# Kernel optimization log

Hardware: AMD Instinct MI355X
Metric: run time of the kernel (lower is better)

Reference implementation:

```python
import jax, jax.numpy as jnp
import numpy as np

B, S, I, H, P = 4096, 1024, 6, 128, 50  # batch, seq_len, input_size, hidden_size, predict_size


def setup_inputs() -> dict:
    key = jax.random.key(0)
    ks = jax.random.split(key, 12)
    k = 1.0 / np.sqrt(H)  # torch LSTM default init: U(-1/sqrt(H), 1/sqrt(H))
    u = lambda kk, shape: jax.random.uniform(kk, shape, jnp.float32, -k, k)
    # xavier_uniform for fc: bound = sqrt(6/(fan_in+fan_out))
    xb = np.sqrt(6.0 / (H + I))
    return {
        "x": jax.random.normal(ks[0], (B, S, I), jnp.float32),
        "w_ih0": u(ks[1], (4 * H, I)),
        "w_hh0": u(ks[2], (4 * H, H)),
        "b_ih0": u(ks[3], (4 * H,)),
        "b_hh0": u(ks[4], (4 * H,)),
        "w_ih1": u(ks[5], (4 * H, H)),
        "w_hh1": u(ks[6], (4 * H, H)),
        "b_ih1": u(ks[7], (4 * H,)),
        "b_hh1": u(ks[8], (4 * H,)),
        "fc_w": jax.random.uniform(ks[9], (I, H), jnp.float32, -xb, xb),
        "fc_b": jnp.full((I,), 0.01, jnp.float32),
    }


def _cell(xt, h, c, w_ih, w_hh, b):
    # gates: [i, f, g, o] stacked along last dim (torch order)
    g = xt @ w_ih.T + h @ w_hh.T + b
    i, f, gg, o = jnp.split(g, 4, axis=-1)
    c = jax.nn.sigmoid(f) * c + jax.nn.sigmoid(i) * jnp.tanh(gg)
    h = jax.nn.sigmoid(o) * jnp.tanh(c)
    return h, c


def reference(x, w_ih0, w_hh0, b_ih0, b_hh0, w_ih1, w_hh1, b_ih1, b_hh1, fc_w, fc_b):
    b0 = b_ih0 + b_hh0
    b1 = b_ih1 + b_hh1
    z = jnp.zeros((x.shape[0], H), x.dtype)

    def two_layer_step(carry, xt):
        h0, c0, h1, c1 = carry
        h0, c0 = _cell(xt, h0, c0, w_ih0, w_hh0, b0)
        h1, c1 = _cell(h0, h1, c1, w_ih1, w_hh1, b1)
        return (h0, c0, h1, c1), None

    # encode the input sequence; last top-layer output == final h1
    (h0, c0, h1, c1), _ = jax.lax.scan(two_layer_step, (z, z, z, z),
                                       jnp.swapaxes(x, 0, 1))  # (S,B,I)
    cur = jnp.tanh(h1 @ fc_w.T + fc_b)  # (B, I)

    def ar_step(carry, _):
        h0, c0, h1, c1, cur = carry
        h0, c0 = _cell(cur, h0, c0, w_ih0, w_hh0, b0)
        h1, c1 = _cell(h0, h1, c1, w_ih1, w_hh1, b1)
        pred = jnp.tanh(h1 @ fc_w.T + fc_b)
        return (h0, c0, h1, c1, pred), pred

    _, preds = jax.lax.scan(ar_step, (h0, c0, h1, c1, cur), None, length=P)
    return jnp.swapaxes(preds, 0, 1)  # (B, P, I)
```

## Files before the change

kernel.cpp:

```cpp
#include <hip/hip_runtime.h>

#define SEQ 1024
#define ISZ 6
#define HSZ 128
#define PRED 50
#define MROW 16
#define HP   136
#define FP   132
#define XSLOT 180

using f32x4  = __attribute__((ext_vector_type(4))) float;
using bf16x8 = __attribute__((ext_vector_type(8))) short;

__device__ __forceinline__ short f2bf(float f){
  union { float f; unsigned u; } v; v.f = f;
  unsigned r = v.u + 0x7FFFu + ((v.u >> 16) & 1u);
  return (short)(r >> 16);
}
__device__ __forceinline__ float sigf(float x){
  float e = __builtin_amdgcn_exp2f(x * -1.4426950408889634f);
  return __builtin_amdgcn_rcpf(1.0f + e);
}
__device__ __forceinline__ float tanhf_(float x){
  float e = __builtin_amdgcn_exp2f(x * 2.8853900817779268f);
  return 1.0f - 2.0f * __builtin_amdgcn_rcpf(1.0f + e);
}

#define PIN(v) asm volatile("" : "+v"(v))

__global__
__attribute__((amdgpu_flat_work_group_size(512, 512)))
void lstm_ar(
    const float* __restrict__ x,
    const float* __restrict__ w_ih0, const float* __restrict__ w_hh0,
    const float* __restrict__ b_ih0, const float* __restrict__ b_hh0,
    const float* __restrict__ w_ih1, const float* __restrict__ w_hh1,
    const float* __restrict__ b_ih1, const float* __restrict__ b_hh1,
    const float* __restrict__ fc_w, const float* __restrict__ fc_b,
    float* __restrict__ out)
{
  __shared__ short s_h0[2][MROW*HP];
  __shared__ short s_h1[2][MROW*HP];
  __shared__ short s_x[XSLOT*MROW*8];
  __shared__ short s_wih0[512*8];
  __shared__ float s_h1f[MROW*FP];
  __shared__ float s_fcw[ISZ*HSZ];
  __shared__ float s_fcb[8];
  __shared__ short s_zpad[8];

  const int tid  = threadIdx.x;
  const int wv   = tid >> 6;
  const int lane = tid & 63;
  const int l15  = lane & 15;
  const int lq   = lane >> 4;
  const int U    = wv * 16;
  const int u    = U + l15;
  const int row0 = blockIdx.x * MROW;

  {
    short* p0 = &s_h0[0][0];
    short* p1 = &s_h1[0][0];
    for (int i = tid; i < 2*MROW*HP; i += 512){ p0[i] = 0; p1[i] = 0; }
    for (int i = tid; i < 65*MROW*8; i += 512) s_x[i] = 0;
    if (tid < 8){ s_zpad[tid] = 0; s_fcb[tid] = (tid < 6) ? fc_b[tid] : 0.f; }
    for (int i = tid; i < ISZ*HSZ; i += 512) s_fcw[i] = fc_w[i];
    {
      #pragma unroll
      for (int k = 0; k < 6; k++) s_wih0[tid*8 + k] = f2bf(w_ih0[tid*6 + k]);
      s_wih0[tid*8 + 6] = 0; s_wih0[tid*8 + 7] = 0;
    }
  }

  bf16x8 whh0f[4][4], wih1f[4][4], whh1f[4][4];
  float bias0[4], bias1[4];
  #pragma unroll
  for (int g = 0; g < 4; g++){
    const int c = g*128 + u;
    bias0[g] = b_ih0[c] + b_hh0[c];
    bias1[g] = b_ih1[c] + b_hh1[c];
    #pragma unroll
    for (int kt = 0; kt < 4; kt++){
      const int off = c*HSZ + kt*32 + lq*8;
      bf16x8 r0, r1, r2;
      #pragma unroll
      for (int i = 0; i < 8; i++){
        r0[i] = f2bf(w_hh0[off + i]);
        r1[i] = f2bf(w_ih1[off + i]);
        r2[i] = f2bf(w_hh1[off + i]);
      }
      whh0f[g][kt] = r0; wih1f[g][kt] = r1; whh1f[g][kt] = r2;
    }
  }

  float c0[4] = {0.f,0.f,0.f,0.f}, c1[4] = {0.f,0.f,0.f,0.f};
  __syncthreads();

  for (int t = 0; t < SEQ + PRED; ++t){
    #pragma unroll
    for (int g = 0; g < 4; g++){
      #pragma unroll
      for (int kt = 0; kt < 4; kt++){
        PIN(whh0f[g][kt]); PIN(wih1f[g][kt]); PIN(whh1f[g][kt]);
      }
    }

    if (t < SEQ && (t & 63) == 0){
      for (int i = tid; i < MROW*64*ISZ; i += 512){
        const int r   = i / (64*ISZ);
        const int rem = i % (64*ISZ);
        const int ts  = rem / ISZ;
        const int k   = rem % ISZ;
        const float v = x[(size_t)(row0 + r)*(SEQ*ISZ) + (size_t)(t + ts)*ISZ + k];
        s_x[(ts*MROW + r)*8 + k] = f2bf(v);
      }
      __syncthreads();
    }
    const int tt = (t < SEQ) ? (t & 63) : 64;
    const int pb = t & 1, qb = pb ^ 1;

    const short* pax = (lq == 0) ? (s_x + (tt*MROW + l15)*8) : s_zpad;
    const bf16x8 ax = *(const bf16x8*)pax;

    f32x4 acc[4];
    #pragma unroll
    for (int g = 0; g < 4; g++){
      const short* pw = (lq == 0) ? (s_wih0 + (g*128 + u)*8) : s_zpad;
      const bf16x8 bw = *(const bf16x8*)pw;
      f32x4 ci; ci[0] = bias0[g]; ci[1] = bias0[g]; ci[2] = bias0[g]; ci[3] = bias0[g];
      acc[g] = __builtin_amdgcn_mfma_f32_16x16x32_bf16(ax, bw, ci, 0, 0, 0);
    }
    #pragma unroll
    for (int kt = 0; kt < 4; kt++){
      const int s = kt*4 + lq;
      const short* pa = s_h0[qb] + l15*HP + s*8;
      const bf16x8 a = *(const bf16x8*)pa;
      #pragma unroll
      for (int g = 0; g < 4; g++)
        acc[g] = __builtin_amdgcn_mfma_f32_16x16x32_bf16(a, whh0f[g][kt], acc[g], 0, 0, 0);
    }
    #pragma unroll
    for (int j = 0; j < 4; j++){
      const float iv = sigf(acc[0][j]);
      const float fv = sigf(acc[1][j]);
      const float gv = tanhf_(acc[2][j]);
      const float ov = sigf(acc[3][j]);
      c0[j] = fv*c0[j] + iv*gv;
      const float h = ov * tanhf_(c0[j]);
      const int r = lq*4 + j;
      s_h0[pb][r*HP + u] = f2bf(h);
    }
    __syncthreads();

    #pragma unroll
    for (int g = 0; g < 4; g++){
      acc[g][0] = bias1[g]; acc[g][1] = bias1[g]; acc[g][2] = bias1[g]; acc[g][3] = bias1[g];
    }
    #pragma unroll
    for (int kt = 0; kt < 4; kt++){
      const int s = kt*4 + lq;
      const short* pa = s_h0[pb] + l15*HP + s*8;
      const bf16x8 a = *(const bf16x8*)pa;
      #pragma unroll
      for (int g = 0; g < 4; g++)
        acc[g] = __builtin_amdgcn_mfma_f32_16x16x32_bf16(a, wih1f[g][kt], acc[g], 0, 0, 0);
    }
    #pragma unroll
    for (int kt = 0; kt < 4; kt++){
      const int s = kt*4 + lq;
      const short* pa = s_h1[qb] + l15*HP + s*8;
      const bf16x8 a = *(const bf16x8*)pa;
      #pragma unroll
      for (int g = 0; g < 4; g++)
        acc[g] = __builtin_amdgcn_mfma_f32_16x16x32_bf16(a, whh1f[g][kt], acc[g], 0, 0, 0);
    }
    const bool dofc = (t >= SEQ - 1);
    #pragma unroll
    for (int j = 0; j < 4; j++){
      const float iv = sigf(acc[0][j]);
      const float fv = sigf(acc[1][j]);
      const float gv = tanhf_(acc[2][j]);
      const float ov = sigf(acc[3][j]);
      c1[j] = fv*c1[j] + iv*gv;
      const float h = ov * tanhf_(c1[j]);
      const int r = lq*4 + j;
      s_h1[pb][r*HP + u] = f2bf(h);
      if (dofc) s_h1f[r*FP + u] = h;
    }
    __syncthreads();

    if (dofc){
      if (tid < 96){
        const int r  = tid / 6;
        const int ii = tid % 6;
        const f32x4* hv = (const f32x4*)(s_h1f + r*FP);
        const f32x4* wf = (const f32x4*)(s_fcw + ii*128);
        float sacc = 0.f;
        #pragma unroll
        for (int kk = 0; kk < 32; kk++){
          const f32x4 a = hv[kk], b = wf[kk];
          sacc += a[0]*b[0] + a[1]*b[1] + a[2]*b[2] + a[3]*b[3];
        }
        const float pred = tanhf_(s_fcb[ii] + sacc);
        s_x[(64*MROW + r)*8 + ii] = f2bf(pred);
        if (t >= SEQ)
          out[(size_t)(row0 + r)*(PRED*ISZ) + (size_t)(t - SEQ)*ISZ + ii] = pred;
      }
      __syncthreads();
    }
  }
}

extern "C" void kernel_launch(void* const* d_in, const int* in_sizes, int n_in,
                              void* d_out, int out_size, void* d_ws, size_t ws_size,
                              hipStream_t stream) {
  const float* x     = (const float*)d_in[0];
  const float* w_ih0 = (const float*)d_in[1];
  const float* w_hh0 = (const float*)d_in[2];
  const float* b_ih0 = (const float*)d_in[3];
  const float* b_hh0 = (const float*)d_in[4];
  const float* w_ih1 = (const float*)d_in[5];
  const float* w_hh1 = (const float*)d_in[6];
  const float* b_ih1 = (const float*)d_in[7];
  const float* b_hh1 = (const float*)d_in[8];
  const float* fc_w  = (const float*)d_in[9];
  const float* fc_b  = (const float*)d_in[10];
  float* out = (float*)d_out;

  const int Btot = in_sizes[0] / (SEQ * ISZ);
  const int nblk = Btot / MROW;

  lstm_ar<<<dim3(nblk), dim3(512), 0, stream>>>(
      x, w_ih0, w_hh0, b_ih0, b_hh0, w_ih1, w_hh1, b_ih1, b_hh1, fc_w, fc_b, out);
}
```

Baseline: 3.675 ms.

## Move LSTM recurrent weights out of registers into LDS and workspace

Only w_ih1 stays register-resident. w_hh1 is converted to bf16 and stored in a 128 KB XOR-swizzled LDS array read on every step. w_hh0 is pre-converted to bf16 in a global workspace and re-streamed each step, with a fallback that reconverts from fp32 when no workspace is available. Biases move to LDS, the x staging chunk shrinks from 64 to 8 steps, and the FC reads bf16 h1 from LDS with fc_w from global. The aim is to cut register pressure, at the cost of extra LDS and global traffic on the serial critical path, a single-buffered h1 that needs an added barrier each step, and lower FC precision.

Result: faster. 3.207 ms (-12.7%).

```diff
diff --git a/kernel.cpp b/kernel.cpp
--- a/kernel.cpp
+++ b/kernel.cpp
@@ -6,8 +6,8 @@
 #define PRED 50
 #define MROW 16
 #define HP   136
-#define FP   132
-#define XSLOT 180
+#define XCH  8
+#define WSB  131072
 
 using f32x4  = __attribute__((ext_vector_type(4))) float;
 using bf16x8 = __attribute__((ext_vector_type(8))) short;
@@ -17,6 +17,9 @@
   unsigned r = v.u + 0x7FFFu + ((v.u >> 16) & 1u);
   return (short)(r >> 16);
 }
+__device__ __forceinline__ float bf2f(unsigned short us){
+  union { unsigned u; float f; } v; v.u = ((unsigned)us) << 16; return v.f;
+}
 __device__ __forceinline__ float sigf(float x){
   float e = __builtin_amdgcn_exp2f(x * -1.4426950408889634f);
   return __builtin_amdgcn_rcpf(1.0f + e);
@@ -28,6 +31,7 @@
 
 #define PIN(v) asm volatile("" : "+v"(v))
 
+template<int PRECVT>
 __global__
 __attribute__((amdgpu_flat_work_group_size(512, 512)))
 void lstm_ar(
@@ -37,14 +41,14 @@
     const float* __restrict__ w_ih1, const float* __restrict__ w_hh1,
     const float* __restrict__ b_ih1, const float* __restrict__ b_hh1,
     const float* __restrict__ fc_w, const float* __restrict__ fc_b,
-    float* __restrict__ out)
+    float* __restrict__ out, unsigned short* __restrict__ wsb)
 {
+  __shared__ short s_whh1[65536];
   __shared__ short s_h0[2][MROW*HP];
-  __shared__ short s_h1[2][MROW*HP];
-  __shared__ short s_x[XSLOT*MROW*8];
+  __shared__ short s_h1[MROW*HP];
+  __shared__ short s_x[(XCH+1)*MROW*8];
   __shared__ short s_wih0[512*8];
-  __shared__ float s_h1f[MROW*FP];
-  __shared__ float s_fcw[ISZ*HSZ];
+  __shared__ float s_bias[2*512];
   __shared__ float s_fcb[8];
   __shared__ short s_zpad[8];
 
@@ -53,90 +57,111 @@
   const int lane = tid & 63;
   const int l15  = lane & 15;
   const int lq   = lane >> 4;
-  const int U    = wv * 16;
-  const int u    = U + l15;
+  const int u    = wv*16 + l15;
   const int row0 = blockIdx.x * MROW;
-
+  char* const whh1b = (char*)s_whh1;
+
+  for (int i = tid; i < 2*MROW*HP; i += 512) (&s_h0[0][0])[i] = 0;
+  for (int i = tid; i < MROW*HP;   i += 512) s_h1[i] = 0;
+  for (int i = tid; i < (XCH+1)*MROW*8; i += 512) s_x[i] = 0;
+  if (tid < 8){ s_zpad[tid] = 0; s_fcb[tid] = (tid < 6) ? fc_b[tid] : 0.f; }
   {
-    short* p0 = &s_h0[0][0];
-    short* p1 = &s_h1[0][0];
-    for (int i = tid; i < 2*MROW*HP; i += 512){ p0[i] = 0; p1[i] = 0; }
-    for (int i = tid; i < 65*MROW*8; i += 512) s_x[i] = 0;
-    if (tid < 8){ s_zpad[tid] = 0; s_fcb[tid] = (tid < 6) ? fc_b[tid] : 0.f; }
-    for (int i = tid; i < ISZ*HSZ; i += 512) s_fcw[i] = fc_w[i];
-    {
-      #pragma unroll
-      for (int k = 0; k < 6; k++) s_wih0[tid*8 + k] = f2bf(w_ih0[tid*6 + k]);
-      s_wih0[tid*8 + 6] = 0; s_wih0[tid*8 + 7] = 0;
-    }
-  }
-
-  bf16x8 whh0f[4][4], wih1f[4][4], whh1f[4][4];
-  float bias0[4], bias1[4];
+    #pragma unroll
+    for (int k = 0; k < 6; k++) s_wih0[tid*8 + k] = f2bf(w_ih0[tid*6 + k]);
+    s_wih0[tid*8 + 6] = 0; s_wih0[tid*8 + 7] = 0;
+  }
+  for (int i = tid; i < 1024; i += 512)
+    s_bias[i] = (i < 512) ? (b_ih0[i] + b_hh0[i]) : (b_ih1[i-512] + b_hh1[i-512]);
+
+  for (int i = tid; i < 32768; i += 512){
+    const int c = i >> 6, kp = i & 63;
+    const unsigned lo = (unsigned short)f2bf(w_hh1[c*128 + 2*kp]);
+    const unsigned hi = (unsigned short)f2bf(w_hh1[c*128 + 2*kp + 1]);
+    *(unsigned*)(whh1b + ((i*4) ^ ((c & 7) << 4))) = lo | (hi << 16);
+  }
+
+  if (PRECVT){
+    #pragma unroll
+    for (int g = 0; g < 4; g++){
+      const int c = g*128 + u;
+      #pragma unroll
+      for (int kt = 0; kt < 4; kt++){
+        const float* wp = w_hh0 + c*HSZ + kt*32 + lq*8;
+        bf16x8 f;
+        #pragma unroll
+        for (int i = 0; i < 8; i++) f[i] = f2bf(wp[i]);
+        *(bf16x8*)(wsb + (((wv*4 + g)*4 + kt)*64 + lane)*8) = f;
+      }
+    }
+  }
+
+  bf16x8 wih1f[4][4];
   #pragma unroll
   for (int g = 0; g < 4; g++){
     const int c = g*128 + u;
-    bias0[g] = b_ih0[c] + b_hh0[c];
-    bias1[g] = b_ih1[c] + b_hh1[c];
-    #pragma unroll
-    for (int kt = 0; kt < 4; kt++){
-      const int off = c*HSZ + kt*32 + lq*8;
-      bf16x8 r0, r1, r2;
-      #pragma unroll
-      for (int i = 0; i < 8; i++){
-        r0[i] = f2bf(w_hh0[off + i]);
-        r1[i] = f2bf(w_ih1[off + i]);
-        r2[i] = f2bf(w_hh1[off + i]);
-      }
-      whh0f[g][kt] = r0; wih1f[g][kt] = r1; whh1f[g][kt] = r2;
+    #pragma unroll
+    for (int kt = 0; kt < 4; kt++){
+      const float* wp = w_ih1 + c*HSZ + kt*32 + lq*8;
+      bf16x8 f;
+      #pragma unroll
+      for (int i = 0; i < 8; i++) f[i] = f2bf(wp[i]);
+      wih1f[g][kt] = f;
     }
   }
 
   float c0[4] = {0.f,0.f,0.f,0.f}, c1[4] = {0.f,0.f,0.f,0.f};
+  volatile const float* vb = s_bias;
   __syncthreads();
 
   for (int t = 0; t < SEQ + PRED; ++t){
     #pragma unroll
     for (int g = 0; g < 4; g++){
       #pragma unroll
-      for (int kt = 0; kt < 4; kt++){
-        PIN(whh0f[g][kt]); PIN(wih1f[g][kt]); PIN(whh1f[g][kt]);
-      }
-    }
-
-    if (t < SEQ && (t & 63) == 0){
-      for (int i = tid; i < MROW*64*ISZ; i += 512){
-        const int r   = i / (64*ISZ);
-        const int rem = i % (64*ISZ);
-        const int ts  = rem / ISZ;
-        const int k   = rem % ISZ;
-        const float v = x[(size_t)(row0 + r)*(SEQ*ISZ) + (size_t)(t + ts)*ISZ + k];
-        s_x[(ts*MROW + r)*8 + k] = f2bf(v);
+      for (int kt = 0; kt < 4; kt++) PIN(wih1f[g][kt]);
+    }
+
+    if (t < SEQ && (t & (XCH-1)) == 0){
+      for (int i = tid; i < XCH*MROW*ISZ; i += 512){
+        const int r = i / (XCH*ISZ), rem = i % (XCH*ISZ);
+        const int ts = rem / ISZ, k = rem % ISZ;
+        s_x[(ts*MROW + r)*8 + k] =
+          f2bf(x[(size_t)(row0 + r)*(SEQ*ISZ) + (size_t)(t + ts)*ISZ + k]);
       }
       __syncthreads();
     }
-    const int tt = (t < SEQ) ? (t & 63) : 64;
+    const int tt = (t < SEQ) ? (t & (XCH-1)) : XCH;
     const int pb = t & 1, qb = pb ^ 1;
 
-    const short* pax = (lq == 0) ? (s_x + (tt*MROW + l15)*8) : s_zpad;
-    const bf16x8 ax = *(const bf16x8*)pax;
-
+    const bf16x8 ax = *(const bf16x8*)((lq == 0) ? (s_x + (tt*MROW + l15)*8) : s_zpad);
     f32x4 acc[4];
     #pragma unroll
     for (int g = 0; g < 4; g++){
-      const short* pw = (lq == 0) ? (s_wih0 + (g*128 + u)*8) : s_zpad;
-      const bf16x8 bw = *(const bf16x8*)pw;
-      f32x4 ci; ci[0] = bias0[g]; ci[1] = bias0[g]; ci[2] = bias0[g]; ci[3] = bias0[g];
+      const bf16x8 bw = *(const bf16x8*)((lq == 0) ? (s_wih0 + (g*128 + u)*8) : s_zpad);
+      const float bg = vb[g*128 + u];
+      f32x4 ci; ci[0] = bg; ci[1] = bg; ci[2] = bg; ci[3] = bg;
       acc[g] = __builtin_amdgcn_mfma_f32_16x16x32_bf16(ax, bw, ci, 0, 0, 0);
     }
     #pragma unroll
     for (int kt = 0; kt < 4; kt++){
-      const int s = kt*4 + lq;
-      const short* pa = s_h0[qb] + l15*HP + s*8;
-      const bf16x8 a = *(const bf16x8*)pa;
+      bf16x8 stg[4];
+      if (PRECVT){
+        #pragma unroll
+        for (int g = 0; g < 4; g++)
+          stg[g] = *(const bf16x8*)(wsb + (((wv*4 + g)*4 + kt)*64 + lane)*8);
+      } else {
+        #pragma unroll
+        for (int g = 0; g < 4; g++){
+          const float* wp = w_hh0 + (g*128 + u)*HSZ + kt*32 + lq*8;
+          bf16x8 f;
+          #pragma unroll
+          for (int i = 0; i < 8; i++) f[i] = f2bf(wp[i]);
+          stg[g] = f;
+        }
+      }
+      const bf16x8 a = *(const bf16x8*)(s_h0[qb] + l15*HP + (kt*4 + lq)*8);
       #pragma unroll
       for (int g = 0; g < 4; g++)
-        acc[g] = __builtin_amdgcn_mfma_f32_16x16x32_bf16(a, whh0f[g][kt], acc[g], 0, 0, 0);
+        acc[g] = __builtin_amdgcn_mfma_f32_16x16x32_bf16(a, stg[g], acc[g], 0, 0, 0);
     }
     #pragma unroll
     for (int j = 0; j < 4; j++){
@@ -146,33 +171,34 @@
       const float ov = sigf(acc[3][j]);
       c0[j] = fv*c0[j] + iv*gv;
       const float h = ov * tanhf_(c0[j]);
-      const int r = lq*4 + j;
-      s_h0[pb][r*HP + u] = f2bf(h);
+      s_h0[pb][(lq*4 + j)*HP + u] = f2bf(h);
     }
     __syncthreads();
 
     #pragma unroll
     for (int g = 0; g < 4; g++){
-      acc[g][0] = bias1[g]; acc[g][1] = bias1[g]; acc[g][2] = bias1[g]; acc[g][3] = bias1[g];
-    }
-    #pragma unroll
-    for (int kt = 0; kt < 4; kt++){
-      const int s = kt*4 + lq;
-      const short* pa = s_h0[pb] + l15*HP + s*8;
-      const bf16x8 a = *(const bf16x8*)pa;
+      const float bg = vb[512 + g*128 + u];
+      acc[g][0] = bg; acc[g][1] = bg; acc[g][2] = bg; acc[g][3] = bg;
+    }
+    #pragma unroll
+    for (int kt = 0; kt < 4; kt++){
+      const bf16x8 a = *(const bf16x8*)(s_h0[pb] + l15*HP + (kt*4 + lq)*8);
       #pragma unroll
       for (int g = 0; g < 4; g++)
         acc[g] = __builtin_amdgcn_mfma_f32_16x16x32_bf16(a, wih1f[g][kt], acc[g], 0, 0, 0);
     }
     #pragma unroll
     for (int kt = 0; kt < 4; kt++){
-      const int s = kt*4 + lq;
-      const short* pa = s_h1[qb] + l15*HP + s*8;
-      const bf16x8 a = *(const bf16x8*)pa;
-      #pragma unroll
-      for (int g = 0; g < 4; g++)
-        acc[g] = __builtin_amdgcn_mfma_f32_16x16x32_bf16(a, whh1f[g][kt], acc[g], 0, 0, 0);
-    }
+      const bf16x8 a = *(const bf16x8*)(s_h1 + l15*HP + (kt*4 + lq)*8);
+      #pragma unroll
+      for (int g = 0; g < 4; g++){
+        const int c = g*128 + u;
+        const bf16x8 b = *(const bf16x8*)(whh1b +
+            ((c*256 + (kt*4 + lq)*16) ^ ((u & 7) << 4)));
+        acc[g] = __builtin_amdgcn_mfma_f32_16x16x32_bf16(a, b, acc[g], 0, 0, 0);
+      }
+    }
+    __syncthreads();
     const bool dofc = (t >= SEQ - 1);
     #pragma unroll
     for (int j = 0; j < 4; j++){
@@ -182,26 +208,19 @@
       const float ov = sigf(acc[3][j]);
       c1[j] = fv*c1[j] + iv*gv;
       const float h = ov * tanhf_(c1[j]);
-      const int r = lq*4 + j;
-      s_h1[pb][r*HP + u] = f2bf(h);
-      if (dofc) s_h1f[r*FP + u] = h;
-    }
-    __syncthreads();
+      s_h1[(lq*4 + j)*HP + u] = f2bf(h);
+    }
 
     if (dofc){
+      __syncthreads();
       if (tid < 96){
-        const int r  = tid / 6;
-        const int ii = tid % 6;
-        const f32x4* hv = (const f32x4*)(s_h1f + r*FP);
-        const f32x4* wf = (const f32x4*)(s_fcw + ii*128);
+        const int r = tid / 6, ii = tid % 6;
         float sacc = 0.f;
-        #pragma unroll
-        for (int kk = 0; kk < 32; kk++){
-          const f32x4 a = hv[kk], b = wf[kk];
-          sacc += a[0]*b[0] + a[1]*b[1] + a[2]*b[2] + a[3]*b[3];
-        }
+        #pragma unroll 4
+        for (int kk = 0; kk < 128; kk++)
+          sacc += bf2f((unsigned short)s_h1[r*HP + kk]) * fc_w[ii*128 + kk];
         const float pred = tanhf_(s_fcb[ii] + sacc);
-        s_x[(64*MROW + r)*8 + ii] = f2bf(pred);
+        s_x[(XCH*MROW + r)*8 + ii] = f2bf(pred);
         if (t >= SEQ)
           out[(size_t)(row0 + r)*(PRED*ISZ) + (size_t)(t - SEQ)*ISZ + ii] = pred;
       }
@@ -225,10 +244,17 @@
   const float* fc_w  = (const float*)d_in[9];
   const float* fc_b  = (const float*)d_in[10];
   float* out = (float*)d_out;
+  unsigned short* wsb = (unsigned short*)d_ws;
 
   const int Btot = in_sizes[0] / (SEQ * ISZ);
   const int nblk = Btot / MROW;
 
-  lstm_ar<<<dim3(nblk), dim3(512), 0, stream>>>(
-      x, w_ih0, w_hh0, b_ih0, b_hh0, w_ih1, w_hh1, b_ih1, b_hh1, fc_w, fc_b, out);
-}
+  if (ws_size >= (size_t)WSB)
+    lstm_ar<1><<<dim3(nblk), dim3(512), 0, stream>>>(
+        x, w_ih0, w_hh0, b_ih0, b_hh0, w_ih1, w_hh1, b_ih1, b_hh1,
+        fc_w, fc_b, out, wsb);
+  else
+    lstm_ar<0><<<dim3(nblk), dim3(512), 0, stream>>>(
+        x, w_ih0, w_hh0, b_ih0, b_hh0, w_ih1, w_hh1, b_ih1, b_hh1,
+        fc_w, fc_b, out, wsb);
+}
```
